# Kernel tuning notes

Hardware: AMD Instinct MI355X
Metric: run time of the kernel (lower is better)

Reference implementation:

```python
import jax, jax.numpy as jnp
import numpy as np

EPS = 1e-8  # torch cosine_similarity norm clamp
TEMP = 1.0

def _gelu(h):
    return jax.nn.gelu(h, approximate=False)  # torch nn.GELU default (erf)

def _layernorm(h, g, b, eps=1e-5):
    mu = jnp.mean(h, axis=-1, keepdims=True)
    var = jnp.var(h, axis=-1, keepdims=True)
    return (h - mu) * jax.lax.rsqrt(var + eps) * g + b

def _encoder(h, eW1, eb1, eW2, eb2, eW3, eb3, ln_g, ln_b):
    h = _gelu(h @ eW1 + eb1)
    h = _gelu(h @ eW2 + eb2)
    h = h @ eW3 + eb3
    return _layernorm(h, ln_g, ln_b)

def _normalize(v):
    n = jnp.sqrt(jnp.sum(v * v, axis=-1, keepdims=True))
    return v / jnp.maximum(n, EPS)

def setup_inputs() -> dict:
    key = jax.random.key(0)
    ks = jax.random.split(key, 8)
    B, D, H, K = 16384, 512, 512, 11
    s = 0.02
    return {
        'x': jax.random.normal(ks[0], (B, D), jnp.float32),
        'tW1': jax.random.normal(ks[1], (K, D, H), jnp.float32) * s,
        'tb1': jnp.zeros((K, H), jnp.float32),
        'tW2': jax.random.normal(ks[2], (K, H, H), jnp.float32) * s,
        'tb2': jnp.zeros((K, H), jnp.float32),
        'tW3': jax.random.normal(ks[3], (K, H, D), jnp.float32) * s,
        'tb3': jnp.zeros((K, D), jnp.float32),
        'eW1': jax.random.normal(ks[4], (D, H), jnp.float32) * s,
        'eb1': jnp.zeros((H,), jnp.float32),
        'eW2': jax.random.normal(ks[5], (H, H), jnp.float32) * s,
        'eb2': jnp.zeros((H,), jnp.float32),
        'eW3': jax.random.normal(ks[6], (H, H), jnp.float32) * s,
        'eb3': jnp.zeros((H,), jnp.float32),
        'ln_g': jnp.ones((H,), jnp.float32),
        'ln_b': jnp.zeros((H,), jnp.float32),
    }

def reference(x, tW1, tb1, tW2, tb2, tW3, tb3, eW1, eb1, eW2, eb2, eW3, eb3, ln_g, ln_b):
    K = tW1.shape[0]
    # K learned transforms, vectorized over k: [K, B, D]
    h = _gelu(jnp.einsum('bi,kij->kbj', x, tW1) + tb1[:, None, :])
    h = _gelu(jnp.einsum('kbi,kij->kbj', h, tW2) + tb2[:, None, :])
    tx = jnp.einsum('kbi,kij->kbj', h, tW3) + tb3[:, None, :]
    # shared encoder on x and on each transformed view
    z = _encoder(x, eW1, eb1, eW2, eb2, eW3, eb3, ln_g, ln_b)      # [B, H]
    zk = _encoder(tx, eW1, eb1, eW2, eb2, eW3, eb3, ln_g, ln_b)    # [K, B, H]
    zn = _normalize(z)
    zkn = _normalize(zk)
    pos = jnp.einsum('bh,kbh->kb', zn, zkn) / TEMP                 # sim(z, z_k)
    S = jnp.einsum('lbh,kbh->lkb', zkn, zkn) / TEMP                # sim(z_l, z_k)
    diag = jnp.eye(K, dtype=bool)[:, :, None]
    Sm = jnp.where(diag, -jnp.inf, S)                              # drop l == k
    all_terms = jnp.concatenate([pos[None], Sm], axis=0)           # [K+1, K, B]
    log_den = jax.nn.logsumexp(all_terms, axis=0)                  # [K, B]
    return -jnp.sum(pos - log_den, axis=0)                         # [B]
```

## Files before the change

### kernel.cpp

```cpp
#include <hip/hip_runtime.h>
#include <hip/hip_bf16.h>
#include <cstdint>

typedef __attribute__((ext_vector_type(8))) short short8;
typedef __attribute__((ext_vector_type(4))) float f32x4;
typedef __attribute__((ext_vector_type(4))) short short4v;

__device__ __forceinline__ float b2f(short s) {
    unsigned u = ((unsigned)(unsigned short)s) << 16;
    return __builtin_bit_cast(float, u);
}
__device__ __forceinline__ short f2b(float f) {
    unsigned u = __builtin_bit_cast(unsigned, f);
    u += 0x7fff + ((u >> 16) & 1);
    return (short)(u >> 16);
}

__device__ __forceinline__ float gelu_t(float x) {
    const float c1 = 2.302184829f;
    const float c2 = 0.102947246f;
    float x2 = x * x;
    float t  = __builtin_fmaf(c2, x2, c1);
    float e  = __builtin_amdgcn_exp2f(x * t);
    return x - __fdividef(x, e + 1.0f);
}

__device__ __forceinline__ void async16(const void* g, void* l) {
    __builtin_amdgcn_global_load_lds(
        (const __attribute__((address_space(1))) unsigned int*)g,
        (__attribute__((address_space(3))) unsigned int*)l, 16, 0, 0);
}

#define NT 8

template<bool GELU>
__global__ __launch_bounds__(512, 2)
void gemm_bt(const short* __restrict__ A, long sA,
             const short* __restrict__ Bt, long sB,
             const float* __restrict__ bias, long sBias,
             short* __restrict__ C, long sC) {
    const int z = blockIdx.z;
    A    += (long)z * sA;
    Bt   += (long)z * sB;
    bias += (long)z * sBias;
    C    += (long)z * sC;

    const int nwg = (int)gridDim.x;
    const int bx  = (int)blockIdx.x;
    int flat = bx;
    if ((nwg & 7) == 0) { const int q = nwg >> 3; flat = (bx & 7) * q + (bx >> 3); }
    const long arow0 = (long)(flat >> 1) * 256;
    const long brow0 = (long)(flat & 1) * 256;

    __shared__ alignas(16) short smem[2 * 2 * 256 * 64];

    const int tid  = threadIdx.x;
    const int lane = tid & 63;
    const int w    = tid >> 6;
    const int wrow = w >> 2, wcol = w & 3;
    const int lr = lane & 15, hi = lane >> 4;

    f32x4 acc[8][4] = {};

    const int srow = lane >> 3;
    const int sc   = ((lane & 7) ^ srow) * 8;

    auto stage = [&](int q, int t) {
        short* Ab = smem + q * 32768;
        short* Bb = Ab + 16384;
        const int k0 = t * 64;
#pragma unroll
        for (int j = 0; j < 4; ++j) {
            const int rbase = j * 64 + w * 8;
            async16(A  + (arow0 + rbase + srow) * 512 + k0 + sc, Ab + rbase * 64);
            async16(Bt + (brow0 + rbase + srow) * 512 + k0 + sc, Bb + rbase * 64);
        }
    };

    stage(0, 0);

    int buf = 0;
#pragma unroll
    for (int t = 0; t < NT; ++t) {
        if (t + 1 < NT) {
            stage(buf ^ 1, t + 1);
            asm volatile("s_waitcnt vmcnt(8)" ::: "memory");
        } else {
            asm volatile("s_waitcnt vmcnt(0)" ::: "memory");
        }
        __builtin_amdgcn_sched_barrier(0);
        __builtin_amdgcn_s_barrier();
        __builtin_amdgcn_sched_barrier(0);

        const short* Ab = smem + buf * 32768;
        const short* Bb = Ab + 16384;
#pragma unroll
        for (int ks = 0; ks < 2; ++ks) {
            const int ch = ks * 4 + hi;
            short8 a[8], b[4];
#pragma unroll
            for (int n = 0; n < 4; ++n) {
                const int r = wcol * 64 + n * 16 + lr;
                b[n] = *(const short8*)&Bb[r * 64 + ((ch ^ (r & 7)) * 8)];
            }
#pragma unroll
            for (int m = 0; m < 8; ++m) {
                const int r = wrow * 128 + m * 16 + lr;
                a[m] = *(const short8*)&Ab[r * 64 + ((ch ^ (r & 7)) * 8)];
            }
            __builtin_amdgcn_s_setprio(1);
#pragma unroll
            for (int m = 0; m < 8; ++m)
#pragma unroll
                for (int n = 0; n < 4; ++n)
                    acc[m][n] = __builtin_amdgcn_mfma_f32_16x16x32_bf16(
                        a[m], b[n], acc[m][n], 0, 0, 0);
            __builtin_amdgcn_s_setprio(0);
        }

        __builtin_amdgcn_s_barrier();
        buf ^= 1;
    }

    short* E = smem + w * (32 * 72);
    const int cl = lr, rl = hi * 4;
#pragma unroll
    for (int h = 0; h < 4; ++h) {
#pragma unroll
        for (int n = 0; n < 4; ++n) {
            const int col = (int)brow0 + wcol * 64 + n * 16 + cl;
            const float bs = bias[col];
            const int ecol = n * 16 + cl;
#pragma unroll
            for (int ml = 0; ml < 2; ++ml) {
                const int m = h * 2 + ml;
                float g0 = acc[m][n][0] + bs, g1 = acc[m][n][1] + bs;
                float g2 = acc[m][n][2] + bs, g3 = acc[m][n][3] + bs;
                if (GELU) { g0 = gelu_t(g0); g1 = gelu_t(g1); g2 = gelu_t(g2); g3 = gelu_t(g3); }
                unsigned p01, p23;
                asm("v_cvt_pk_bf16_f32 %0, %1, %2" : "=v"(p01) : "v"(g0), "v"(g1));
                asm("v_cvt_pk_bf16_f32 %0, %1, %2" : "=v"(p23) : "v"(g2), "v"(g3));
                const int r0 = ml * 16 + rl;
                E[(r0 + 0) * 72 + ecol] = (short)(p01 & 0xffff);
                E[(r0 + 1) * 72 + ecol] = (short)(p01 >> 16);
                E[(r0 + 2) * 72 + ecol] = (short)(p23 & 0xffff);
                E[(r0 + 3) * 72 + ecol] = (short)(p23 >> 16);
            }
        }
#pragma unroll
        for (int chunk = 0; chunk < 4; ++chunk) {
            const int rloc = chunk * 8 + (lane >> 3);
            const int c0   = (lane & 7) * 8;
            short8 v = *(const short8*)&E[rloc * 72 + c0];
            *(short8*)&C[(arow0 + wrow * 128 + h * 32 + rloc) * 512
                         + brow0 + wcol * 64 + c0] = v;
        }
    }
}

__global__ __launch_bounds__(256)
void transpose_conv(const float* __restrict__ src, short* __restrict__ dst) {
    __shared__ float t[32][33];
    const long moff = (long)blockIdx.z * 512 * 512;
    const float* s = src + moff;
    short* d = dst + moff;
    const int tx = threadIdx.x & 31, ty = threadIdx.x >> 5;
    const int bi = blockIdx.x, bj = blockIdx.y;
#pragma unroll
    for (int j = 0; j < 4; ++j)
        t[ty + j * 8][tx] = s[(long)(bi * 32 + ty + j * 8) * 512 + bj * 32 + tx];
    __syncthreads();
#pragma unroll
    for (int j = 0; j < 4; ++j)
        d[(long)(bj * 32 + ty + j * 8) * 512 + bi * 32 + tx] = f2b(t[tx][ty + j * 8]);
}

__global__ __launch_bounds__(256)
void conv_f32_bf16(const float* __restrict__ src, short* __restrict__ dst, long n) {
    long i = ((long)blockIdx.x * 256 + threadIdx.x) * 4;
    if (i >= n) return;
    float4 f = *(const float4*)&src[i];
    short4v o;
    o[0] = f2b(f.x); o[1] = f2b(f.y); o[2] = f2b(f.z); o[3] = f2b(f.w);
    *(short4v*)&dst[i] = o;
}

__global__ __launch_bounds__(256)
void bias_fold(const float* __restrict__ tb3, const short* __restrict__ wtE1,
               const float* __restrict__ eb1, float* __restrict__ bB) {
    const int wid = threadIdx.x >> 6, lane = threadIdx.x & 63;
    const int idx = blockIdx.x * 4 + wid;
    const int k = idx >> 9, n = idx & 511;
    short8 wv = *(const short8*)&wtE1[(long)n * 512 + lane * 8];
    const float* tb = tb3 + (long)k * 512 + lane * 8;
    float s = 0.f;
#pragma unroll
    for (int j = 0; j < 8; ++j) s += b2f(wv[j]) * tb[j];
#pragma unroll
    for (int o = 1; o < 64; o <<= 1) s += __shfl_xor(s, o, 64);
    if (lane == 0) bB[(long)(k + 1) * 512 + n] = s + eb1[n];
}

__global__ __launch_bounds__(256)
void ln_loss(const short* __restrict__ H, const float* __restrict__ g,
             const float* __restrict__ bta, float* __restrict__ out, int CH) {
    __shared__ alignas(16) short Z[4][16 * 520];
    const int wid = threadIdx.x >> 6, lane = threadIdx.x & 63;
    const long b = (long)blockIdx.x * 4 + wid;
    short* Zw = &Z[wid][0];

#pragma unroll
    for (int r = 12; r < 16; ++r)
        *(short8*)&Zw[r * 520 + lane * 8] = (short8){0, 0, 0, 0, 0, 0, 0, 0};

    for (int s = 0; s < 12; ++s) {
        short8 t = *(const short8*)&H[((long)s * CH + b) * 512 + lane * 8];
        float v[8];
        float sum = 0.f, ss = 0.f;
#pragma unroll
        for (int j = 0; j < 8; ++j) { v[j] = b2f(t[j]); sum += v[j]; ss += v[j] * v[j]; }
#pragma unroll
        for (int o = 1; o < 64; o <<= 1) { sum += __shfl_xor(sum, o, 64); ss += __shfl_xor(ss, o, 64); }
        const float mu = sum * (1.f / 512.f);
        const float rs = rsqrtf(ss * (1.f / 512.f) - mu * mu + 1e-5f);
        float y[8]; float nsq = 0.f;
#pragma unroll
        for (int j = 0; j < 8; ++j) {
            const int col = lane * 8 + j;
            y[j] = (v[j] - mu) * rs * g[col] + bta[col];
            nsq += y[j] * y[j];
        }
#pragma unroll
        for (int o = 1; o < 64; o <<= 1) nsq += __shfl_xor(nsq, o, 64);
        const float inv = 1.f / fmaxf(sqrtf(nsq), 1e-8f);
        short8 o8;
#pragma unroll
        for (int j = 0; j < 8; ++j) o8[j] = f2b(y[j] * inv);
        *(short8*)&Zw[s * 520 + lane * 8] = o8;
    }

    f32x4 acc = {0.f, 0.f, 0.f, 0.f};
    const int lr = lane & 15, hi = lane >> 4;
#pragma unroll
    for (int st = 0; st < 16; ++st) {
        short8 a = *(const short8*)&Zw[lr * 520 + st * 32 + hi * 8];
        acc = __builtin_amdgcn_mfma_f32_16x16x32_bf16(a, a, acc, 0, 0, 0);
    }
    const int col = lr;
    float lmax = -3.0e38f;
    bool valid[4];
#pragma unroll
    for (int i = 0; i < 4; ++i) {
        const int row = hi * 4 + i;
        valid[i] = (row < 12) && (row != col);
        if (valid[i]) lmax = fmaxf(lmax, acc[i]);
    }
    lmax = fmaxf(lmax, __shfl_xor(lmax, 16, 64));
    lmax = fmaxf(lmax, __shfl_xor(lmax, 32, 64));
    float esum = 0.f;
#pragma unroll
    for (int i = 0; i < 4; ++i)
        if (valid[i]) esum += __builtin_amdgcn_exp2f((acc[i] - lmax) * 1.44269504f);
    esum += __shfl_xor(esum, 16, 64);
    esum += __shfl_xor(esum, 32, 64);
    float contrib = 0.f;
    if (hi == 0 && col >= 1 && col <= 11) {
        const float logden = lmax + __builtin_amdgcn_logf(esum) * 0.6931471806f;
        contrib = acc[0] - logden;
    }
#pragma unroll
    for (int o = 1; o < 16; o <<= 1) contrib += __shfl_xor(contrib, o, 64);
    if (lane == 0) out[b] = -contrib;
}

extern "C" void kernel_launch(void* const* d_in, const int* in_sizes, int n_in,
                              void* d_out, int out_size, void* d_ws, size_t ws_size,
                              hipStream_t stream) {
    const float* x    = (const float*)d_in[0];
    const float* tW1  = (const float*)d_in[1];
    const float* tb1  = (const float*)d_in[2];
    const float* tW2  = (const float*)d_in[3];
    const float* tb2  = (const float*)d_in[4];
    const float* tW3  = (const float*)d_in[5];
    const float* tb3  = (const float*)d_in[6];
    const float* eW1  = (const float*)d_in[7];
    const float* eb1  = (const float*)d_in[8];
    const float* eW2  = (const float*)d_in[9];
    const float* eb2  = (const float*)d_in[10];
    const float* eW3  = (const float*)d_in[11];
    const float* eb3  = (const float*)d_in[12];
    const float* ln_g = (const float*)d_in[13];
    const float* ln_b = (const float*)d_in[14];

    const int  B    = in_sizes[0] / 512;
    const long WMAT = 512L * 512L;

    int  c  = 1;
    long CH = B;
    for (;;) {
        CH = (long)B / c;
        size_t need = (size_t)48 * WMAT * 2 + (512 + 12 * 512) * 4
                    + (size_t)24 * CH * 512 * 2 + 8192;
        if (need <= ws_size || CH <= 256) break;
        c <<= 1;
    }
    const long SLAB = 12L * CH * 512;

    short* wt   = (short*)d_ws;
    short* Mt   = wt + 36L * WMAT;
    float* zero512 = (float*)(Mt + 12L * WMAT);
    float* bB   = zero512 + 512;
    short* S    = (short*)(bB + 12 * 512);
    short* T    = S + SLAB;

    {
        dim3 tgK(16, 16, 11), tg1(16, 16, 1);
        transpose_conv<<<tgK, 256, 0, stream>>>(tW1, wt + 0L * WMAT);
        transpose_conv<<<tgK, 256, 0, stream>>>(tW2, wt + 11L * WMAT);
        conv_f32_bf16<<<(unsigned)((11 * WMAT / 4 + 255) / 256), 256, 0, stream>>>(
            tW3, wt + 22L * WMAT, 11 * WMAT);
        transpose_conv<<<tg1, 256, 0, stream>>>(eW1, wt + 33L * WMAT);
        transpose_conv<<<tg1, 256, 0, stream>>>(eW2, wt + 34L * WMAT);
        transpose_conv<<<tg1, 256, 0, stream>>>(eW3, wt + 35L * WMAT);

        hipMemsetAsync(zero512, 0, 512 * sizeof(float), stream);
        gemm_bt<false><<<dim3(4, 1, 11), 512, 0, stream>>>(
            wt + 33L * WMAT, 0, wt + 22L * WMAT, WMAT, zero512, 0, Mt + WMAT, WMAT);
        hipMemcpyAsync(Mt, wt + 33L * WMAT, WMAT * sizeof(short),
                       hipMemcpyDeviceToDevice, stream);
        hipMemcpyAsync(bB, eb1, 512 * sizeof(float),
                       hipMemcpyDeviceToDevice, stream);
        bias_fold<<<(11 * 512) / 4, 256, 0, stream>>>(tb3, wt + 33L * WMAT, eb1, bB);
    }

    const long SC = CH * 512;
    const dim3 gT((unsigned)(CH / 256 * 2), 1, 11);
    const dim3 gF((unsigned)(CH / 256 * 2), 1, 12);
    const dim3 gE((unsigned)(12 * CH / 256 * 2), 1, 1);

    for (int ch = 0; ch < c; ++ch) {
        conv_f32_bf16<<<(unsigned)((SC / 4 + 255) / 256), 256, 0, stream>>>(
            x + (long)ch * SC, S, SC);

        gemm_bt<true ><<<gT, 512, 0, stream>>>(S, 0,  wt + 0L * WMAT,  WMAT, tb1, 512, T + SC, SC);
        gemm_bt<true ><<<gT, 512, 0, stream>>>(T + SC, SC, wt + 11L * WMAT, WMAT, tb2, 512, S + SC, SC);
        gemm_bt<true ><<<gF, 512, 0, stream>>>(S, SC, Mt, WMAT, bB, 512, T, SC);
        gemm_bt<true ><<<gE, 512, 0, stream>>>(T, 0, wt + 34L * WMAT, 0, eb2, 0, S, 0);
        gemm_bt<false><<<gE, 512, 0, stream>>>(S, 0, wt + 35L * WMAT, 0, eb3, 0, T, 0);

        ln_loss<<<(unsigned)(CH / 4), 256, 0, stream>>>(
            T, ln_g, ln_b, (float*)d_out + (long)ch * CH, (int)CH);
    }
}
```

Before: 911.2 us.

## Restructure GEMM main loop into finer-grained half-K stages with interleaved prefetch

After: 987.4 us. 1.08x slower.

```diff
diff --git a/kernel.cpp b/kernel.cpp
--- a/kernel.cpp
+++ b/kernel.cpp
@@ -31,10 +31,10 @@
         (__attribute__((address_space(3))) unsigned int*)l, 16, 0, 0);
 }
 
-#define NT 8
+#define VMW(N) asm volatile("s_waitcnt vmcnt(" #N ")" ::: "memory")
 
 template<bool GELU>
-__global__ __launch_bounds__(512, 2)
+__global__ __launch_bounds__(512)
 void gemm_bt(const short* __restrict__ A, long sA,
              const short* __restrict__ Bt, long sB,
              const float* __restrict__ bias, long sBias,
@@ -52,7 +52,7 @@
     const long arow0 = (long)(flat >> 1) * 256;
     const long brow0 = (long)(flat & 1) * 256;
 
-    __shared__ alignas(16) short smem[2 * 2 * 256 * 64];
+    __shared__ alignas(16) short smem[2 * 32768];
 
     const int tid  = threadIdx.x;
     const int lane = tid & 63;
@@ -62,64 +62,74 @@
 
     f32x4 acc[8][4] = {};
 
-    const int srow = lane >> 3;
-    const int sc   = ((lane & 7) ^ srow) * 8;
-
-    auto stage = [&](int q, int t) {
-        short* Ab = smem + q * 32768;
-        short* Bb = Ab + 16384;
-        const int k0 = t * 64;
-#pragma unroll
-        for (int j = 0; j < 4; ++j) {
-            const int rbase = j * 64 + w * 8;
-            async16(A  + (arow0 + rbase + srow) * 512 + k0 + sc, Ab + rbase * 64);
-            async16(Bt + (brow0 + rbase + srow) * 512 + k0 + sc, Bb + rbase * 64);
+    auto stageH = [&](int st, int sks, int sB_) {
+        short* reg = smem + (st & 1) * 32768 + (sB_ ? 16384 : 0) + sks * 8192;
+        const short* srcb = sB_ ? Bt : A;
+        const long r0g = sB_ ? brow0 : arow0;
+        const int kc = st * 64 + sks * 32;
+#pragma unroll
+        for (int jj = 0; jj < 2; ++jj) {
+            const int R = w * 32 + jj * 16;
+            const int row = R + (lane >> 2);
+            const int gc = (lane & 3) ^ ((row >> 1) & 3);
+            async16(srcb + (r0g + row) * 512 + kc + gc * 8, reg + R * 32);
         }
     };
 
-    stage(0, 0);
-
-    int buf = 0;
-#pragma unroll
-    for (int t = 0; t < NT; ++t) {
-        if (t + 1 < NT) {
-            stage(buf ^ 1, t + 1);
-            asm volatile("s_waitcnt vmcnt(8)" ::: "memory");
-        } else {
-            asm volatile("s_waitcnt vmcnt(0)" ::: "memory");
-        }
-        __builtin_amdgcn_sched_barrier(0);
-        __builtin_amdgcn_s_barrier();
-        __builtin_amdgcn_sched_barrier(0);
-
-        const short* Ab = smem + buf * 32768;
-        const short* Bb = Ab + 16384;
-#pragma unroll
-        for (int ks = 0; ks < 2; ++ks) {
-            const int ch = ks * 4 + hi;
-            short8 a[8], b[4];
+    stageH(0, 0, 0); stageH(0, 0, 1);
+    stageH(0, 1, 0); stageH(0, 1, 1);
+    stageH(1, 0, 0); stageH(1, 0, 1);
+    VMW(8);
+    __builtin_amdgcn_sched_barrier(0);
+    __builtin_amdgcn_s_barrier();
+    __builtin_amdgcn_sched_barrier(0);
+
+#pragma unroll
+    for (int i = 0; i < 4; ++i) {
+#pragma unroll
+        for (int p = 0; p < 8; ++p) {
+            const int tau = 2 * i + (p >> 2);
+            const int ks  = (p >> 1) & 1;
+            const int mh  = p & 1;
+            const short* Ar = smem + (tau & 1) * 32768 + ks * 8192;
+            const short* Br = Ar + 16384;
+            short8 a[4], b[4];
 #pragma unroll
             for (int n = 0; n < 4; ++n) {
-                const int r = wcol * 64 + n * 16 + lr;
-                b[n] = *(const short8*)&Bb[r * 64 + ((ch ^ (r & 7)) * 8)];
+                const int row = wcol * 64 + n * 16 + lr;
+                b[n] = *(const short8*)&Br[row * 32 + ((hi ^ ((row >> 1) & 3)) << 3)];
             }
 #pragma unroll
-            for (int m = 0; m < 8; ++m) {
-                const int r = wrow * 128 + m * 16 + lr;
-                a[m] = *(const short8*)&Ab[r * 64 + ((ch ^ (r & 7)) * 8)];
+            for (int j = 0; j < 4; ++j) {
+                const int row = wrow * 128 + (mh * 4 + j) * 16 + lr;
+                a[j] = *(const short8*)&Ar[row * 32 + ((hi ^ ((row >> 1) & 3)) << 3)];
             }
+            {
+                const int st  = (p < 2) ? 2 * i + 1 : (p < 6) ? 2 * i + 2 : 2 * i + 3;
+                const int sks = (p < 2) ? 1 : (p < 4) ? 0 : (p < 6) ? 1 : 0;
+                const int sB_ = p & 1;
+                if (st < 8) stageH(st, sks, sB_);
+            }
+            if (i < 3) { VMW(8); }
+            else if (p < 3) { VMW(8); }
+            else if (p < 5) { VMW(4); }
+            else { VMW(0); }
+            __builtin_amdgcn_sched_barrier(0);
+            __builtin_amdgcn_s_barrier();
+            __builtin_amdgcn_sched_barrier(0);
+            asm volatile("s_waitcnt lgkmcnt(0)" ::: "memory");
+            __builtin_amdgcn_sched_barrier(0);
             __builtin_amdgcn_s_setprio(1);
 #pragma unroll
-            for (int m = 0; m < 8; ++m)
+            for (int j = 0; j < 4; ++j)
 #pragma unroll
                 for (int n = 0; n < 4; ++n)
-                    acc[m][n] = __builtin_amdgcn_mfma_f32_16x16x32_bf16(
-                        a[m], b[n], acc[m][n], 0, 0, 0);
+                    acc[mh * 4 + j][n] = __builtin_amdgcn_mfma_f32_16x16x32_bf16(
+                        a[j], b[n], acc[mh * 4 + j][n], 0, 0, 0);
             __builtin_amdgcn_s_setprio(0);
-        }
-
-        __builtin_amdgcn_s_barrier();
-        buf ^= 1;
+            __builtin_amdgcn_s_barrier();
+            __builtin_amdgcn_sched_barrier(0);
+        }
     }
 
     short* E = smem + w * (32 * 72);
```
